# Kernel optimization log

Measured on AMD Instinct MI355X. Metric: run time of the kernel, lower is better.

## Reference

```python
import jax, jax.numpy as jnp
import numpy as np

B, N, H, NB, NCT = 8, 4096, 1024, 128, 33
LN_EPS = 1e-5


def setup_inputs() -> dict:
    key = jax.random.key(0)
    ks = jax.random.split(key, 12)
    x = jax.random.normal(ks[0], (B, N, H), dtype=jnp.float32)
    cancer_type = jax.random.randint(ks[1], (B,), 0, NCT)
    block_ids = jax.random.randint(ks[2], (B, N), 0, NB)
    pad_mask = jnp.zeros((B, N), dtype=bool)
    s1 = 1.0 / np.sqrt(H)
    s2 = 1.0 / np.sqrt(H // 2)
    return {
        "x": x,
        "cancer_type": cancer_type,
        "block_ids": block_ids,
        "pad_mask": pad_mask,
        "W1": jax.random.normal(ks[3], (H, H // 2), jnp.float32) * s1,
        "b1": jnp.zeros((H // 2,), jnp.float32),
        "W2": jax.random.normal(ks[4], (H // 2, 1), jnp.float32) * s2,
        "b2": jnp.zeros((1,), jnp.float32),
        "ct_emb": jax.random.normal(ks[5], (NCT, NB), jnp.float32) * 0.1,
        "Wp": jax.random.normal(ks[6], (H, H), jnp.float32) * s1,
        "bp": jnp.zeros((H,), jnp.float32),
        "ln_g": jnp.ones((H,), jnp.float32),
        "ln_b": jnp.zeros((H,), jnp.float32),
    }


def reference(x, cancer_type, block_ids, pad_mask, W1, b1, W2, b2, ct_emb, Wp, bp, ln_g, ln_b):
    nb = ct_emb.shape[1]
    # gate MLP: (B,N)
    h = jnp.tanh(x @ W1 + b1)
    gate = (h @ W2 + b2)[..., 0]
    valid = ~pad_mask
    # block membership mask (B, NB, N)
    mask = (block_ids[:, None, :] == jnp.arange(nb)[None, :, None]) & valid[:, None, :]
    neg_inf = jnp.float32(-jnp.inf)
    scores = jnp.where(mask, gate[:, None, :], neg_inf)
    # stable masked softmax over N; empty blocks -> all-zero weights (nan_to_num(0))
    m = jnp.max(scores, axis=-1, keepdims=True)
    m = jnp.where(jnp.isfinite(m), m, 0.0)
    e = jnp.where(mask, jnp.exp(scores - m), 0.0)
    denom = jnp.sum(e, axis=-1, keepdims=True)
    w = jnp.where(denom > 0, e / jnp.maximum(denom, 1e-30), 0.0)
    # cancer-type modulation: weights * (1 + 0.1*ct_mod[:,bid])
    ct_mod = ct_emb[cancer_type]  # (B, NB)
    w = w * (1.0 + 0.1 * ct_mod)[:, :, None]
    # pooled per-block token (B, NB, H)
    pooled = jnp.einsum('bkn,bnh->bkh', w, x)
    # block_proj: Linear -> LayerNorm -> ELU (dropout = eval identity)
    y = pooled @ Wp + bp
    mu = jnp.mean(y, axis=-1, keepdims=True)
    var = jnp.mean((y - mu) ** 2, axis=-1, keepdims=True)
    y = (y - mu) * jax.lax.rsqrt(var + LN_EPS) * ln_g + ln_b
    y = jax.nn.elu(y)
    has_b = jnp.any(mask, axis=-1)              # (B, NB)
    present = jnp.any(has_b, axis=0)            # (NB,) torch loop skips blocks absent everywhere
    block_tokens = jnp.where(present[None, :, None], y, 0.0)
    return block_tokens, has_b
```

## Files before the change

### kernel.cpp

```cpp
#include <hip/hip_runtime.h>

#define NTOK 4096
#define HDIM 1024
#define HHALF 512
#define NBLK 128
#define CAP 256
#define XELEMS 33554432ull

typedef __attribute__((ext_vector_type(8))) short short8;
typedef __attribute__((ext_vector_type(4))) float f32x4;
typedef short bf16s;

__device__ __forceinline__ short f2bf(float f) {
    unsigned u = __builtin_bit_cast(unsigned, f);
    u = (u + 0x7fffu + ((u >> 16) & 1u)) >> 16;
    return (short)u;
}
__device__ __forceinline__ void gload_lds16(const void* g, void* l) {
    __builtin_amdgcn_global_load_lds(
        (const __attribute__((address_space(1))) unsigned int*)g,
        (__attribute__((address_space(3))) unsigned int*)l, 16, 0, 0);
}
__device__ __forceinline__ float fast_tanh(float v) {
    float e = __expf(2.0f * v);
    return 1.0f - 2.0f / (e + 1.0f);
}

__global__ void k_xcvt(const float* __restrict__ in, bf16s* __restrict__ out) {
    for (size_t i = ((size_t)blockIdx.x * 256 + threadIdx.x) * 8; i < XELEMS;
         i += (size_t)gridDim.x * 256 * 8) {
        float4 a = *reinterpret_cast<const float4*>(&in[i]);
        float4 b = *reinterpret_cast<const float4*>(&in[i + 4]);
        short h[8] = {f2bf(a.x), f2bf(a.y), f2bf(a.z), f2bf(a.w),
                      f2bf(b.x), f2bf(b.y), f2bf(b.z), f2bf(b.w)};
        *reinterpret_cast<int4*>(&out[i]) = *reinterpret_cast<const int4*>(h);
    }
}

__global__ void k_tcvt2(const float* __restrict__ W1, const float* __restrict__ Wp,
                        bf16s* __restrict__ w1t, bf16s* __restrict__ wpt) {
    __shared__ float tile[64][65];
    const int by = blockIdx.y;
    const float* in = (by < 8) ? W1 : Wp;
    bf16s* out = (by < 8) ? w1t : wpt;
    const int Nc = (by < 8) ? HHALF : HDIM;
    const int n0 = ((by < 8) ? by : (by - 8)) * 64;
    const int k0 = blockIdx.x * 64;
    const int tx = threadIdx.x & 63, ty = threadIdx.x >> 6;
    #pragma unroll
    for (int i = 0; i < 16; ++i) {
        int r = ty + i * 4;
        tile[r][tx] = in[(size_t)(k0 + r) * Nc + n0 + tx];
    }
    __syncthreads();
    #pragma unroll
    for (int i = 0; i < 16; ++i) {
        int r = ty + i * 4;
        out[(size_t)(n0 + r) * 1024 + k0 + tx] = f2bf(tile[tx][r]);
    }
}

__global__ __launch_bounds__(256, 2) void k_gemm_g(
    const bf16s* __restrict__ xb, const bf16s* __restrict__ w1t,
    const float* __restrict__ b1, const float* __restrict__ w2,
    float* __restrict__ partial)
{
    __shared__ alignas(16) bf16s As[2][128 * 64];
    __shared__ alignas(16) bf16s Bs[2][128 * 64];
    __shared__ float gp[2][128];

    const int tid = threadIdx.x;
    const int lane = tid & 63;
    const int wv = tid >> 6;
    const int wr = wv >> 1, wc = wv & 1;
    const int phys = blockIdx.x;
    const int logical = (phys & 7) * 128 + (phys >> 3);
    const int row0 = (logical >> 2) * 128;
    const int col0 = (logical & 3) * 128;
    const int c0 = lane & 15, khalf = lane >> 4;

    const int srow = wv * 32 + (lane >> 3);
    const int sj   = (lane & 7) ^ (lane >> 3);
    const bf16s* aSrc = &xb [(size_t)(row0 + srow) * HDIM + sj * 8];
    const bf16s* bSrc = &w1t[(size_t)(col0 + srow) * HDIM + sj * 8];
    const int sdst = (wv * 256 + lane) * 8;

    f32x4 acc[4][4] = {};

    #pragma unroll
    for (int q = 0; q < 4; ++q) {
        gload_lds16(aSrc + q * 8 * HDIM, &As[0][sdst + q * 512]);
        gload_lds16(bSrc + q * 8 * HDIM, &Bs[0][sdst + q * 512]);
    }

    for (int t = 0; t < 16; ++t) {
        const int cur = t & 1;
        if (t < 15) {
            const int koff = (t + 1) * 64;
            #pragma unroll
            for (int q = 0; q < 4; ++q) {
                gload_lds16(aSrc + q * 8 * HDIM + koff, &As[cur ^ 1][sdst + q * 512]);
                gload_lds16(bSrc + q * 8 * HDIM + koff, &Bs[cur ^ 1][sdst + q * 512]);
            }
            asm volatile("s_waitcnt vmcnt(8)" ::: "memory");
        } else {
            asm volatile("s_waitcnt vmcnt(0)" ::: "memory");
        }
        __builtin_amdgcn_s_barrier();
        __builtin_amdgcn_sched_barrier(0);

        #pragma unroll
        for (int s = 0; s < 2; ++s) {
            short8 av[4], bv[4];
            #pragma unroll
            for (int mf = 0; mf < 4; ++mf) {
                int ra = wr * 64 + mf * 16 + c0;
                int ka = (s * 4 + khalf) ^ (ra & 7);
                av[mf] = *reinterpret_cast<const short8*>(&As[cur][ra * 64 + ka * 8]);
            }
            #pragma unroll
            for (int nf = 0; nf < 4; ++nf) {
                int rb = wc * 64 + nf * 16 + c0;
                int kb = (s * 4 + khalf) ^ (rb & 7);
                bv[nf] = *reinterpret_cast<const short8*>(&Bs[cur][rb * 64 + kb * 8]);
            }
            #pragma unroll
            for (int nf = 0; nf < 4; ++nf)
                #pragma unroll
                for (int mf = 0; mf < 4; ++mf)
                    acc[mf][nf] = __builtin_amdgcn_mfma_f32_16x16x32_bf16(av[mf], bv[nf], acc[mf][nf], 0, 0, 0);
        }

        asm volatile("s_waitcnt lgkmcnt(0)" ::: "memory");
        __builtin_amdgcn_sched_barrier(0);
        __builtin_amdgcn_s_barrier();
    }

    float b1v[4], w2v[4];
    #pragma unroll
    for (int nf = 0; nf < 4; ++nf) {
        int gc = col0 + wc * 64 + nf * 16 + c0;
        b1v[nf] = b1[gc];
        w2v[nf] = w2[gc];
    }
    #pragma unroll
    for (int mf = 0; mf < 4; ++mf) {
        #pragma unroll
        for (int reg = 0; reg < 4; ++reg) {
            float s = 0.f;
            #pragma unroll
            for (int nf = 0; nf < 4; ++nf)
                s += fast_tanh(acc[mf][nf][reg] + b1v[nf]) * w2v[nf];
            s += __shfl_xor(s, 1); s += __shfl_xor(s, 2);
            s += __shfl_xor(s, 4); s += __shfl_xor(s, 8);
            if (c0 == 0) gp[wc][wr * 64 + mf * 16 + khalf * 4 + reg] = s;
        }
    }
    __syncthreads();
    if (tid < 128)
        partial[(size_t)(logical & 3) * 32768 + row0 + tid] = gp[0][tid] + gp[1][tid];
}

__global__ void k_blocks(const int* __restrict__ block_ids, const unsigned char* __restrict__ pad,
                         const float* __restrict__ part, const float* __restrict__ b2,
                         float* __restrict__ gate, const int* __restrict__ ct,
                         const float* __restrict__ ct_emb,
                         int* __restrict__ counts, float* __restrict__ mblk,
                         float* __restrict__ wscale, int* __restrict__ lists,
                         float* __restrict__ out_hasb)
{
    const int blk = blockIdx.x;
    const int b = blk >> 7, k = blk & 127;
    const int lane = threadIdx.x;
    const int base = b * NTOK;
    const int lbase = blk * CAP;
    const unsigned long long ltmask = (1ull << lane) - 1ull;
    const float b2v = b2[0];

    float m = -__builtin_inff();
    float s = 0.f;
    int pos = 0;
    for (int t0 = 0; t0 < NTOK; t0 += 64) {
        int t = t0 + lane;
        bool mt = (block_ids[base + t] == k) && (pad[base + t] == 0);
        unsigned long long mask = __ballot(mt);
        if (mt) {
            int r = base + t;
            float g = part[r] + part[32768 + r] + part[65536 + r] + part[98304 + r] + b2v;
            gate[r] = g;
            int my = pos + __popcll(mask & ltmask);
            if (my < CAP) lists[lbase + my] = t;
            float mn = fmaxf(m, g);
            s = s * __expf(m - mn) + __expf(g - mn);
            m = mn;
        }
        pos += __popcll(mask);
    }
    #pragma unroll
    for (int off = 1; off < 64; off <<= 1) {
        float om = __shfl_xor(m, off);
        float os = __shfl_xor(s, off);
        float mn = fmaxf(m, om);
        float sa = (m == -__builtin_inff()) ? 0.f : s * __expf(m - mn);
        float sb = (om == -__builtin_inff()) ? 0.f : os * __expf(om - mn);
        s = sa + sb;
        m = mn;
    }
    if (lane == 0) {
        counts[blk] = pos;
        mblk[blk] = (pos > 0) ? m : 0.f;
        float mod = 1.0f + 0.1f * ct_emb[ct[b] * NBLK + k];
        wscale[blk] = (pos > 0 && s > 0.f) ? (mod / fmaxf(s, 1e-30f)) : 0.f;
        out_hasb[blk] = (pos > 0) ? 1.f : 0.f;
    }
}

__global__ void k_pool(const bf16s* __restrict__ xb, const float* __restrict__ gate,
                       const int* __restrict__ lists, const int* __restrict__ counts,
                       const float* __restrict__ mblk, const float* __restrict__ wscale,
                       bf16s* __restrict__ pooled)
{
    const int blk = blockIdx.x;
    const int b = blk >> 7;
    const int tid = threadIdx.x;
    const int base = b * NTOK;
    const int cnt = min(counts[blk], CAP);
    const int lbase = blk * CAP;
    const float m = mblk[blk], ws = wscale[blk];

    float4 acc = {0.f, 0.f, 0.f, 0.f};
    for (int i = 0; i < cnt; ++i) {
        int n = lists[lbase + i];
        float w = __expf(gate[base + n] - m);
        int2 rv = *reinterpret_cast<const int2*>(&xb[(size_t)(base + n) * HDIM + tid * 4]);
        short s4[4];
        *reinterpret_cast<int2*>(s4) = rv;
        unsigned u0 = ((unsigned)(unsigned short)s4[0]) << 16;
        unsigned u1 = ((unsigned)(unsigned short)s4[1]) << 16;
        unsigned u2 = ((unsigned)(unsigned short)s4[2]) << 16;
        unsigned u3 = ((unsigned)(unsigned short)s4[3]) << 16;
        acc.x += w * __builtin_bit_cast(float, u0);
        acc.y += w * __builtin_bit_cast(float, u1);
        acc.z += w * __builtin_bit_cast(float, u2);
        acc.w += w * __builtin_bit_cast(float, u3);
    }
    short o[4] = {f2bf(acc.x * ws), f2bf(acc.y * ws), f2bf(acc.z * ws), f2bf(acc.w * ws)};
    *reinterpret_cast<int2*>(&pooled[(size_t)blk * HDIM + tid * 4]) =
        *reinterpret_cast<const int2*>(o);
}

__global__ __launch_bounds__(256) void k_gemm2(
    const bf16s* __restrict__ pooled, const bf16s* __restrict__ wpt,
    const float* __restrict__ bp, float* __restrict__ y)
{
    __shared__ alignas(16) bf16s As[2][64 * 32];
    __shared__ alignas(16) bf16s Bs[2][64 * 32];
    const int tid = threadIdx.x;
    const int lane = tid & 63;
    const int wv = tid >> 6;
    const int wr = wv >> 1, wc = wv & 1;
    const int row0 = (blockIdx.x >> 4) * 64, col0 = (blockIdx.x & 15) * 64;
    const int c0 = lane & 15, khalf = lane >> 4;

    const int sr = wv * 16 + (lane >> 2);
    const int sj = (lane & 3) ^ ((sr >> 1) & 3);
    const int sdst = (wv * 16) * 32 + lane * 8;
    const bf16s* srcA = &pooled[(size_t)(row0 + sr) * 1024 + sj * 8];
    const bf16s* srcB = &wpt[(size_t)(col0 + sr) * 1024 + sj * 8];

    f32x4 acc[2][2] = {};

    gload_lds16(srcA, &As[0][sdst]);
    gload_lds16(srcB, &Bs[0][sdst]);

    for (int t = 0; t < 32; ++t) {
        const int cur = t & 1;
        if (t < 31) {
            gload_lds16(srcA + (t + 1) * 32, &As[cur ^ 1][sdst]);
            gload_lds16(srcB + (t + 1) * 32, &Bs[cur ^ 1][sdst]);
            asm volatile("s_waitcnt vmcnt(2)" ::: "memory");
        } else {
            asm volatile("s_waitcnt vmcnt(0)" ::: "memory");
        }
        __builtin_amdgcn_s_barrier();
        __builtin_amdgcn_sched_barrier(0);
        #pragma unroll
        for (int mf = 0; mf < 2; ++mf) {
            int ra = wr * 32 + mf * 16 + c0;
            short8 av = *reinterpret_cast<const short8*>(
                &As[cur][ra * 32 + ((khalf ^ ((ra >> 1) & 3)) * 8)]);
            #pragma unroll
            for (int nf = 0; nf < 2; ++nf) {
                int rb = wc * 32 + nf * 16 + c0;
                short8 bv = *reinterpret_cast<const short8*>(
                    &Bs[cur][rb * 32 + ((khalf ^ ((rb >> 1) & 3)) * 8)]);
                acc[mf][nf] = __builtin_amdgcn_mfma_f32_16x16x32_bf16(av, bv, acc[mf][nf], 0, 0, 0);
            }
        }
        asm volatile("s_waitcnt lgkmcnt(0)" ::: "memory");
        __builtin_amdgcn_sched_barrier(0);
        __builtin_amdgcn_s_barrier();
    }
    #pragma unroll
    for (int mf = 0; mf < 2; ++mf)
        #pragma unroll
        for (int nf = 0; nf < 2; ++nf)
            #pragma unroll
            for (int reg = 0; reg < 4; ++reg) {
                int grow = row0 + wr * 32 + mf * 16 + khalf * 4 + reg;
                int gcol = col0 + wc * 32 + nf * 16 + c0;
                y[(size_t)grow * 1024 + gcol] = acc[mf][nf][reg] + bp[gcol];
            }
}

__global__ void k_lnelu(const float* __restrict__ y, const float* __restrict__ ln_g,
                        const float* __restrict__ ln_b, const int* __restrict__ counts,
                        float* __restrict__ outp)
{
    const int row = blockIdx.x;
    const int k = row & 127;
    const int tid = threadIdx.x;

    float4 v = *reinterpret_cast<const float4*>(&y[(size_t)row * 1024 + tid * 4]);
    float s = v.x + v.y + v.z + v.w;
    float ss = v.x * v.x + v.y * v.y + v.z * v.z + v.w * v.w;
    #pragma unroll
    for (int off = 32; off; off >>= 1) { s += __shfl_xor(s, off); ss += __shfl_xor(ss, off); }

    __shared__ float sbuf[4], ssbuf[4];
    int wv = tid >> 6;
    if ((tid & 63) == 0) { sbuf[wv] = s; ssbuf[wv] = ss; }
    __syncthreads();
    s = sbuf[0] + sbuf[1] + sbuf[2] + sbuf[3];
    ss = ssbuf[0] + ssbuf[1] + ssbuf[2] + ssbuf[3];

    float mu = s * (1.f / 1024.f);
    float var = ss * (1.f / 1024.f) - mu * mu;
    float rstd = rsqrtf(var + 1e-5f);

    bool pres = false;
    #pragma unroll
    for (int bb = 0; bb < 8; ++bb) pres = pres || (counts[bb * NBLK + k] > 0);

    float4 g4 = *reinterpret_cast<const float4*>(&ln_g[tid * 4]);
    float4 b4 = *reinterpret_cast<const float4*>(&ln_b[tid * 4]);
    float vals[4] = {v.x, v.y, v.z, v.w};
    float gs[4] = {g4.x, g4.y, g4.z, g4.w};
    float bs[4] = {b4.x, b4.y, b4.z, b4.w};
    float4 o;
    float* op = &o.x;
    #pragma unroll
    for (int j = 0; j < 4; ++j) {
        float t = (vals[j] - mu) * rstd * gs[j] + bs[j];
        t = (t > 0.f) ? t : expm1f(t);
        op[j] = pres ? t : 0.f;
    }
    *reinterpret_cast<float4*>(&outp[(size_t)row * 1024 + tid * 4]) = o;
}

extern "C" void kernel_launch(void* const* d_in, const int* in_sizes, int n_in,
                              void* d_out, int out_size, void* d_ws, size_t ws_size,
                              hipStream_t stream)
{
    const float* x      = (const float*)d_in[0];
    const int*   ct     = (const int*)d_in[1];
    const int*   bids   = (const int*)d_in[2];
    const unsigned char* pad = (const unsigned char*)d_in[3];
    const float* W1     = (const float*)d_in[4];
    const float* b1     = (const float*)d_in[5];
    const float* W2     = (const float*)d_in[6];
    const float* b2     = (const float*)d_in[7];
    const float* ct_emb = (const float*)d_in[8];
    const float* Wp     = (const float*)d_in[9];
    const float* bp     = (const float*)d_in[10];
    const float* ln_g   = (const float*)d_in[11];
    const float* ln_b   = (const float*)d_in[12];
    float* outF = (float*)d_out;

    char* ws = (char*)d_ws;
    bf16s* w1t    = (bf16s*)(ws + 0);
    bf16s* wpt    = (bf16s*)(ws + 1048576);
    float* gate   = (float*)(ws + 3145728);
    float* part   = (float*)(ws + 3276800);
    float* mblk   = (float*)(ws + 3801088);
    float* wscal  = (float*)(ws + 3805184);
    int*   counts = (int*)  (ws + 3809280);
    int*   lists  = (int*)  (ws + 3813376);
    bf16s* pooled = (bf16s*)(ws + 4861952);
    float* ybuf   = (float*)(ws + 6959104);
    bf16s* xb     = (bf16s*)(ws + 11153408);

    k_tcvt2<<<dim3(16, 24), 256, 0, stream>>>(W1, Wp, w1t, wpt);
    k_xcvt<<<2048, 256, 0, stream>>>(x, xb);
    k_gemm_g<<<1024, 256, 0, stream>>>(xb, w1t, b1, W2, part);
    k_blocks<<<1024, 64, 0, stream>>>(bids, pad, part, b2, gate, ct, ct_emb,
                                      counts, mblk, wscal, lists,
                                      outF + (size_t)8 * NBLK * HDIM);
    k_pool<<<1024, 256, 0, stream>>>(xb, gate, lists, counts, mblk, wscal, pooled);
    k_gemm2<<<256, 256, 0, stream>>>(pooled, wpt, bp, ybuf);
    k_lnelu<<<1024, 256, 0, stream>>>(ybuf, ln_g, ln_b, counts, outF);
}
```

Baseline: 148.6 us.

## Enlarge gate GEMM tiles to 256x256 with 8-wave split-phase pipeline

Replaces the 128x128-tile gate GEMM (1024 blocks, 4 waves) with a 256x256-tile version (256 blocks, 8 waves, one block per CU). It uses K=32 LDS stages, interleaves the global-to-LDS loads with two half-MFMA phases, and raises wave priority around the MFMA bursts. The larger tiles cut global and LDS traffic per FLOP, and with only two column tiles the follow-on kernel sums two partials instead of four. The cost is higher register and LDS pressure, a single block per CU, and many more barriers per iteration.

```diff
diff --git a/kernel.cpp b/kernel.cpp
--- a/kernel.cpp
+++ b/kernel.cpp
@@ -60,91 +60,140 @@
     }
 }
 
-__global__ __launch_bounds__(256, 2) void k_gemm_g(
+__global__ __launch_bounds__(512, 1) void k_gemm8(
     const bf16s* __restrict__ xb, const bf16s* __restrict__ w1t,
     const float* __restrict__ b1, const float* __restrict__ w2,
     float* __restrict__ partial)
 {
-    __shared__ alignas(16) bf16s As[2][128 * 64];
-    __shared__ alignas(16) bf16s Bs[2][128 * 64];
-    __shared__ float gp[2][128];
+    __shared__ alignas(16) bf16s As[2][256 * 32];
+    __shared__ alignas(16) bf16s Bs[2][256 * 32];
 
     const int tid = threadIdx.x;
     const int lane = tid & 63;
     const int wv = tid >> 6;
-    const int wr = wv >> 1, wc = wv & 1;
+    const int wm = wv >> 2;
+    const int wn = wv & 3;
     const int phys = blockIdx.x;
-    const int logical = (phys & 7) * 128 + (phys >> 3);
-    const int row0 = (logical >> 2) * 128;
-    const int col0 = (logical & 3) * 128;
+    const int logical = (phys & 7) * 32 + (phys >> 3);
+    const int row0 = (logical >> 1) * 256;
+    const int ct   = logical & 1;
+    const int col0 = ct * 256;
     const int c0 = lane & 15, khalf = lane >> 4;
 
-    const int srow = wv * 32 + (lane >> 3);
-    const int sj   = (lane & 7) ^ (lane >> 3);
-    const bf16s* aSrc = &xb [(size_t)(row0 + srow) * HDIM + sj * 8];
-    const bf16s* bSrc = &w1t[(size_t)(col0 + srow) * HDIM + sj * 8];
-    const int sdst = (wv * 256 + lane) * 8;
-
-    f32x4 acc[4][4] = {};
-
-    #pragma unroll
-    for (int q = 0; q < 4; ++q) {
-        gload_lds16(aSrc + q * 8 * HDIM, &As[0][sdst + q * 512]);
-        gload_lds16(bSrc + q * 8 * HDIM, &Bs[0][sdst + q * 512]);
-    }
-
-    for (int t = 0; t < 16; ++t) {
-        const int cur = t & 1;
-        if (t < 15) {
-            const int koff = (t + 1) * 64;
-            #pragma unroll
-            for (int q = 0; q < 4; ++q) {
-                gload_lds16(aSrc + q * 8 * HDIM + koff, &As[cur ^ 1][sdst + q * 512]);
-                gload_lds16(bSrc + q * 8 * HDIM + koff, &Bs[cur ^ 1][sdst + q * 512]);
-            }
-            asm volatile("s_waitcnt vmcnt(8)" ::: "memory");
+    const int sj = (lane & 3) ^ ((lane >> 3) & 3);
+    const int rA0 = ((wv & 4) ? 128 : 0) + (wv & 3) * 16 + (lane >> 2);
+    const int rB0 = wv * 16 + (lane >> 2);
+    const bf16s* aS0 = &xb [(size_t)(row0 + rA0) * HDIM + sj * 8];
+    const bf16s* aS1 = aS0 + (size_t)64 * HDIM;
+    const bf16s* bS0 = &w1t[(size_t)(col0 + rB0) * HDIM + sj * 8];
+    const bf16s* bS1 = bS0 + (size_t)128 * HDIM;
+    const int adst0 = (((wv & 4) ? 128 : 0) + (wv & 3) * 16) * 32 + lane * 8;
+    const int adst1 = adst0 + 64 * 32;
+    const int bdst0 = (wv * 16) * 32 + lane * 8;
+    const int bdst1 = bdst0 + 128 * 32;
+
+    const int ch8 = (khalf ^ ((c0 >> 1) & 3)) * 8;
+    const int arA = (wm * 128 + c0) * 32 + ch8;
+    const int brB = (wn * 64 + c0) * 32 + ch8;
+
+    f32x4 acc[8][4] = {};
+    short8 bvv[4];
+    short8 av[4];
+
+#define MFMA16(MB)                                                            \
+    __builtin_amdgcn_s_setprio(1);                                           \
+    _Pragma("unroll")                                                         \
+    for (int n = 0; n < 4; ++n)                                               \
+        _Pragma("unroll")                                                     \
+        for (int m = 0; m < 4; ++m)                                           \
+            acc[(MB) + m][n] =                                                \
+                __builtin_amdgcn_mfma_f32_16x16x32_bf16(av[m], bvv[n],        \
+                                                        acc[(MB) + m][n], 0, 0, 0); \
+    __builtin_amdgcn_s_setprio(0);
+
+    gload_lds16(aS0, &As[0][adst0]);
+    gload_lds16(aS1, &As[0][adst1]);
+    gload_lds16(bS0, &Bs[0][bdst0]);
+    gload_lds16(bS1, &Bs[0][bdst1]);
+    gload_lds16(aS0 + 32, &As[1][adst0]);
+    gload_lds16(bS0 + 32, &Bs[1][bdst0]);
+
+    for (int it = 0; it < 16; ++it) {
+        const int ka = 2 * it, kb = 2 * it + 1;
+        const bool nl = (it < 15);
+
+        gload_lds16(aS1 + kb * 32, &As[1][adst1]);
+        gload_lds16(bS1 + kb * 32, &Bs[1][bdst1]);
+        asm volatile("s_waitcnt vmcnt(4)" ::: "memory");
+        __builtin_amdgcn_s_barrier();
+        #pragma unroll
+        for (int m = 0; m < 4; ++m)
+            av[m] = *reinterpret_cast<const short8*>(&As[0][arA + m * 512]);
+        #pragma unroll
+        for (int n = 0; n < 4; ++n)
+            bvv[n] = *reinterpret_cast<const short8*>(&Bs[0][brB + n * 512]);
+        asm volatile("s_waitcnt lgkmcnt(0)" ::: "memory");
+        __builtin_amdgcn_sched_barrier(0);
+        MFMA16(0)
+        __builtin_amdgcn_s_barrier();
+
+        #pragma unroll
+        for (int m = 0; m < 4; ++m)
+            av[m] = *reinterpret_cast<const short8*>(&As[0][arA + (4 + m) * 512]);
+        if (nl) {
+            gload_lds16(aS0 + (ka + 2) * 32, &As[0][adst0]);
+            gload_lds16(bS0 + (ka + 2) * 32, &Bs[0][bdst0]);
+        }
+        __builtin_amdgcn_s_barrier();
+        asm volatile("s_waitcnt lgkmcnt(0)" ::: "memory");
+        __builtin_amdgcn_sched_barrier(0);
+        MFMA16(4)
+        __builtin_amdgcn_s_barrier();
+
+        if (nl) {
+            gload_lds16(aS1 + (ka + 2) * 32, &As[0][adst1]);
+            gload_lds16(bS1 + (ka + 2) * 32, &Bs[0][bdst1]);
+            asm volatile("s_waitcnt vmcnt(4)" ::: "memory");
         } else {
             asm volatile("s_waitcnt vmcnt(0)" ::: "memory");
         }
         __builtin_amdgcn_s_barrier();
-        __builtin_amdgcn_sched_barrier(0);
-
-        #pragma unroll
-        for (int s = 0; s < 2; ++s) {
-            short8 av[4], bv[4];
-            #pragma unroll
-            for (int mf = 0; mf < 4; ++mf) {
-                int ra = wr * 64 + mf * 16 + c0;
-                int ka = (s * 4 + khalf) ^ (ra & 7);
-                av[mf] = *reinterpret_cast<const short8*>(&As[cur][ra * 64 + ka * 8]);
-            }
-            #pragma unroll
-            for (int nf = 0; nf < 4; ++nf) {
-                int rb = wc * 64 + nf * 16 + c0;
-                int kb = (s * 4 + khalf) ^ (rb & 7);
-                bv[nf] = *reinterpret_cast<const short8*>(&Bs[cur][rb * 64 + kb * 8]);
-            }
-            #pragma unroll
-            for (int nf = 0; nf < 4; ++nf)
-                #pragma unroll
-                for (int mf = 0; mf < 4; ++mf)
-                    acc[mf][nf] = __builtin_amdgcn_mfma_f32_16x16x32_bf16(av[mf], bv[nf], acc[mf][nf], 0, 0, 0);
-        }
-
+        #pragma unroll
+        for (int m = 0; m < 4; ++m)
+            av[m] = *reinterpret_cast<const short8*>(&As[1][arA + m * 512]);
+        #pragma unroll
+        for (int n = 0; n < 4; ++n)
+            bvv[n] = *reinterpret_cast<const short8*>(&Bs[1][brB + n * 512]);
         asm volatile("s_waitcnt lgkmcnt(0)" ::: "memory");
         __builtin_amdgcn_sched_barrier(0);
-        __builtin_amdgcn_s_barrier();
-    }
-
+        MFMA16(0)
+        __builtin_amdgcn_s_barrier();
+
+        #pragma unroll
+        for (int m = 0; m < 4; ++m)
+            av[m] = *reinterpret_cast<const short8*>(&As[1][arA + (4 + m) * 512]);
+        if (nl) {
+            gload_lds16(aS0 + (kb + 2) * 32, &As[1][adst0]);
+            gload_lds16(bS0 + (kb + 2) * 32, &Bs[1][bdst0]);
+        }
+        __builtin_amdgcn_s_barrier();
+        asm volatile("s_waitcnt lgkmcnt(0)" ::: "memory");
+        __builtin_amdgcn_sched_barrier(0);
+        MFMA16(4)
+        __builtin_amdgcn_s_barrier();
+    }
+#undef MFMA16
+
+    float* gp = reinterpret_cast<float*>(&As[0][0]);
     float b1v[4], w2v[4];
     #pragma unroll
     for (int nf = 0; nf < 4; ++nf) {
-        int gc = col0 + wc * 64 + nf * 16 + c0;
+        int gc = col0 + wn * 64 + nf * 16 + c0;
         b1v[nf] = b1[gc];
         w2v[nf] = w2[gc];
     }
     #pragma unroll
-    for (int mf = 0; mf < 4; ++mf) {
+    for (int mf = 0; mf < 8; ++mf) {
         #pragma unroll
         for (int reg = 0; reg < 4; ++reg) {
             float s = 0.f;
@@ -153,12 +202,14 @@
                 s += fast_tanh(acc[mf][nf][reg] + b1v[nf]) * w2v[nf];
             s += __shfl_xor(s, 1); s += __shfl_xor(s, 2);
             s += __shfl_xor(s, 4); s += __shfl_xor(s, 8);
-            if (c0 == 0) gp[wc][wr * 64 + mf * 16 + khalf * 4 + reg] = s;
+            if (c0 == 0)
+                gp[wn * 256 + wm * 128 + mf * 16 + khalf * 4 + reg] = s;
         }
     }
     __syncthreads();
-    if (tid < 128)
-        partial[(size_t)(logical & 3) * 32768 + row0 + tid] = gp[0][tid] + gp[1][tid];
+    if (tid < 256)
+        partial[(size_t)ct * 32768 + row0 + tid] =
+            gp[tid] + gp[256 + tid] + gp[512 + tid] + gp[768 + tid];
 }
 
 __global__ void k_blocks(const int* __restrict__ block_ids, const unsigned char* __restrict__ pad,
@@ -186,7 +237,7 @@
         unsigned long long mask = __ballot(mt);
         if (mt) {
             int r = base + t;
-            float g = part[r] + part[32768 + r] + part[65536 + r] + part[98304 + r] + b2v;
+            float g = part[r] + part[32768 + r] + b2v;
             gate[r] = g;
             int my = pos + __popcll(mask & ltmask);
             if (my < CAP) lists[lbase + my] = t;
@@ -392,7 +443,7 @@
 
     k_tcvt2<<<dim3(16, 24), 256, 0, stream>>>(W1, Wp, w1t, wpt);
     k_xcvt<<<2048, 256, 0, stream>>>(x, xb);
-    k_gemm_g<<<1024, 256, 0, stream>>>(xb, w1t, b1, W2, part);
+    k_gemm8<<<256, 512, 0, stream>>>(xb, w1t, b1, W2, part);
     k_blocks<<<1024, 64, 0, stream>>>(bids, pad, part, b2, gate, ct, ct_emb,
                                       counts, mblk, wscal, lists,
                                       outF + (size_t)8 * NBLK * HDIM);
```

Result: faster. 144.3 us (-2.9%).
